# Kernel optimization log

Measured on AMD Instinct MI355X. Metric: run time of the kernel, lower is better.

The kernel has to match this reference:

```python
import jax, jax.numpy as jnp
import numpy as np

PC_RANGE = (-50.0, -50.0, -4.0, 50.0, 50.0, 4.0)
IMG_H, IMG_W = 256.0, 704.0
EPS = 1e-5


def _bilinear_sample(feat, u, v):
    # feat [H,W,C]; u,v [M] in [0,1]; matches F.grid_sample(align_corners=False, padding_mode='zeros')
    H, W, _ = feat.shape
    x = u * W - 0.5
    y = v * H - 0.5
    x0 = jnp.floor(x)
    y0 = jnp.floor(y)
    dx = (x - x0)[:, None]
    dy = (y - y0)[:, None]
    x0 = x0.astype(jnp.int32)
    y0 = y0.astype(jnp.int32)

    def g(xi, yi):
        inb = ((xi >= 0) & (xi < W) & (yi >= 0) & (yi < H)).astype(feat.dtype)[:, None]
        return feat[jnp.clip(yi, 0, H - 1), jnp.clip(xi, 0, W - 1)] * inb

    return (g(x0, y0) * (1 - dx) * (1 - dy) + g(x0 + 1, y0) * dx * (1 - dy)
            + g(x0, y0 + 1) * (1 - dx) * dy + g(x0 + 1, y0 + 1) * dx * dy)


def _conv1x1(t, w, b):
    return jnp.einsum('bchw,oc->bohw', t, w) + b[None, :, None, None]


def _inorm(t, eps=1e-5):
    # InstanceNorm2d (affine=False): normalize per (b, c) over spatial dims
    m = t.mean(axis=(2, 3), keepdims=True)
    var = t.var(axis=(2, 3), keepdims=True)
    return (t - m) * jax.lax.rsqrt(var + eps)


def _forward(feat, lidar2img, bev_pos, pe_w1, pe_b1, pe_w2, pe_b2, pe_w3, pe_b3,
             c1_w, c1_b, c2_w, c2_b, c3_w, c3_b):
    B, N, C, Hf, Wf = feat.shape
    _, P, Hb, Wb, _ = bev_pos.shape
    Q = Hb * Wb
    lo = jnp.asarray(PC_RANGE[:3], feat.dtype)
    hi = jnp.asarray(PC_RANGE[3:], feat.dtype)
    # 'b p h w d -> b (h w) p d', then scale normalized coords into pc_range
    ref01 = jnp.transpose(bev_pos, (0, 2, 3, 1, 4)).reshape(B, Q, P, 3)
    ref = ref01 * (hi - lo) + lo
    # project through per-camera lidar2img (homogeneous)
    pts = jnp.concatenate([ref, jnp.ones_like(ref[..., :1])], axis=-1)  # [B,Q,P,4]
    cam = jnp.einsum('bnij,bqpj->bnqpi', lidar2img, pts)                # [B,N,Q,P,4]
    homo = cam[..., 2]
    z = jnp.maximum(homo, EPS)
    u = cam[..., 0] / z / IMG_W
    v = cam[..., 1] / z / IMG_H
    valid = ((homo > EPS) & (u > 0.0) & (u < 1.0) & (v > 0.0) & (v < 1.0)).astype(feat.dtype)
    # bilinear gather per camera; feats to channel-last ('b n (g c) h w -> (b g) n h w c', G=1)
    fmap = jnp.transpose(feat, (0, 1, 3, 4, 2)).reshape(B * N, Hf, Wf, C)
    samp = jax.vmap(_bilinear_sample)(fmap, u.reshape(B * N, Q * P), v.reshape(B * N, Q * P))
    samp = samp.reshape(B, N, Q, P, C) * valid[..., None]
    samp = samp.sum(axis=1)  # sum over cameras -> [B,Q,P,C]
    # PositionalEncodingMap(3 -> 256 -> 256 -> 128) on normalized reference points
    pe = jax.nn.relu(ref01 @ pe_w1 + pe_b1)
    pe = jax.nn.relu(pe @ pe_w2 + pe_b2)
    pe = pe @ pe_w3 + pe_b3
    samp = samp + pe
    # 'b (h w) g p c -> b (p g c) h w' with g=1
    x = jnp.transpose(samp.reshape(B, Hb, Wb, P, C), (0, 3, 4, 1, 2)).reshape(B, P * C, Hb, Wb)
    gelu = lambda t: jax.nn.gelu(t, approximate=False)
    x = gelu(_inorm(_conv1x1(x, c1_w, c1_b)))
    x = gelu(_inorm(_conv1x1(x, c2_w, c2_b)))
    x = _conv1x1(x, c3_w, c3_b)
    return x


def setup_inputs() -> dict:
    key = jax.random.key(0)
    ks = jax.random.split(key, 16)
    B, N, C, Hf, Wf = 1, 6, 128, 32, 88
    P, Hb, Wb = 4, 160, 160
    E = 128
    MID = 256
    s = 0.02
    return {
        'feat': jax.random.normal(ks[0], (B, N, C, Hf, Wf), jnp.float32),
        'lidar2img': jax.random.normal(ks[1], (B, N, 4, 4), jnp.float32),
        'bev_pos': jax.random.uniform(ks[2], (B, P, Hb, Wb, 3), jnp.float32),
        'pe_w1': jax.random.normal(ks[3], (3, MID), jnp.float32) * s,
        'pe_b1': jnp.zeros((MID,), jnp.float32),
        'pe_w2': jax.random.normal(ks[4], (MID, MID), jnp.float32) * s,
        'pe_b2': jnp.zeros((MID,), jnp.float32),
        'pe_w3': jax.random.normal(ks[5], (MID, E), jnp.float32) * s,
        'pe_b3': jnp.zeros((E,), jnp.float32),
        'c1_w': jax.random.normal(ks[6], (4 * E, P * 128), jnp.float32) * s,
        'c1_b': jnp.zeros((4 * E,), jnp.float32),
        'c2_w': jax.random.normal(ks[7], (E, 4 * E), jnp.float32) * s,
        'c2_b': jnp.zeros((E,), jnp.float32),
        'c3_w': jax.random.normal(ks[8], (E, E), jnp.float32) * s,
        'c3_b': jnp.zeros((E,), jnp.float32),
    }


def reference(feat, lidar2img, bev_pos, pe_w1, pe_b1, pe_w2, pe_b2, pe_w3, pe_b3,
              c1_w, c1_b, c2_w, c2_b, c3_w, c3_b):
    return _forward(feat, lidar2img, bev_pos, pe_w1, pe_b1, pe_w2, pe_b2, pe_w3, pe_b3,
                    c1_w, c1_b, c2_w, c2_b, c3_w, c3_b)
```

## Files before the change

kernel.cpp:

```cpp
#include <hip/hip_runtime.h>
#include <cstdint>
#include <cstddef>

using frag8 = __attribute__((ext_vector_type(8))) short;
using f32x4 = __attribute__((ext_vector_type(4))) float;

__device__ __forceinline__ float b2f_bits(unsigned short u) {
    union { uint32_t u32; float f; } x; x.u32 = ((uint32_t)u) << 16; return x.f;
}
__device__ __forceinline__ float b2f_lo(uint32_t pk) {
    return __builtin_bit_cast(float, pk << 16);
}
__device__ __forceinline__ float b2f_hi(uint32_t pk) {
    return __builtin_bit_cast(float, pk & 0xffff0000u);
}
__device__ __forceinline__ unsigned short f2b(float f) {
    uint32_t u = __builtin_bit_cast(uint32_t, f);
    uint32_t r = (u + 0x7fffu + ((u >> 16) & 1u)) >> 16;
    return (unsigned short)r;
}

#define HF 32
#define WFEAT 88
#define NCAM 6
#define NPT 102400
#define BM 128
#define BN 128
#define BK 64

__global__ __launch_bounds__(256) void k_prep(const float* __restrict__ feat,
                                              const float* __restrict__ pw2,
                                              const float* __restrict__ pw3,
                                              const float* __restrict__ c1w,
                                              const float* __restrict__ c2w,
                                              const float* __restrict__ c3w,
                                              const float* __restrict__ pw1,
                                              const float* __restrict__ pb1,
                                              const float* __restrict__ l2i,
                                              const float* __restrict__ bev,
                                              unsigned short* __restrict__ featT,
                                              unsigned short* __restrict__ W2Tb,
                                              unsigned short* __restrict__ W3Tb,
                                              unsigned short* __restrict__ C1Wb,
                                              unsigned short* __restrict__ C2Wb,
                                              unsigned short* __restrict__ C3Wb,
                                              unsigned short* __restrict__ H1,
                                              float* __restrict__ stats,
                                              int* __restrict__ poff,
                                              float4* __restrict__ pwts) {
    __shared__ unsigned short tile[64 * 132];
    int b = blockIdx.x, t = threadIdx.x;
    if (b < 25600) {
        int idx = b * 256 + t;
        int m = idx >> 6;
        int o4 = (idx & 63) * 4;
        int q = m >> 2, p = m & 3;
        int h = q / 160, w = q - h * 160;
        const float* bv = bev + ((p * 160 + h) * 160 + w) * 3;
        float cx = bv[0], cy = bv[1], cz = bv[2];
        float4 a0 = *(const float4*)(pw1 + o4);
        float4 a1 = *(const float4*)(pw1 + 256 + o4);
        float4 a2 = *(const float4*)(pw1 + 512 + o4);
        float4 bb = *(const float4*)(pb1 + o4);
        ushort4 o;
        o.x = f2b(fmaxf(cx * a0.x + cy * a1.x + cz * a2.x + bb.x, 0.f));
        o.y = f2b(fmaxf(cx * a0.y + cy * a1.y + cz * a2.y + bb.y, 0.f));
        o.z = f2b(fmaxf(cx * a0.z + cy * a1.z + cz * a2.z + bb.z, 0.f));
        o.w = f2b(fmaxf(cx * a0.w + cy * a1.w + cz * a2.w + bb.w, 0.f));
        *(ushort4*)(H1 + (size_t)m * 256 + o4) = o;
        return;
    }
    b -= 25600;
    if (b < 2400) {
        int idx = b * 256 + t;
        int n = idx / NPT, pt = idx - n * NPT;
        int q = pt >> 2, p = pt & 3;
        int h = q / 160, w = q - h * 160;
        const float* bv = bev + ((p * 160 + h) * 160 + w) * 3;
        float rx = bv[0] * 100.f - 50.f;
        float ry = bv[1] * 100.f - 50.f;
        float rz = bv[2] * 8.f - 4.f;
        const float* M = l2i + n * 16;
        float c0   = M[0] * rx + M[1] * ry + M[2]  * rz + M[3];
        float c1v  = M[4] * rx + M[5] * ry + M[6]  * rz + M[7];
        float homo = M[8] * rx + M[9] * ry + M[10] * rz + M[11];
        float z = fmaxf(homo, 1e-5f);
        float u = c0 / z / 704.0f;
        float v = c1v / z / 256.0f;
        if (!(homo > 1e-5f && u > 0.f && u < 1.f && v > 0.f && v < 1.f)) {
            poff[idx] = -1;
            return;
        }
        float fx = u * (float)WFEAT - 0.5f;
        float fy = v * (float)HF - 0.5f;
        float fx0 = floorf(fx), fy0 = floorf(fy);
        float dx = fx - fx0, dy = fy - fy0;
        int x0 = (int)fx0, y0 = (int)fy0;
        float wxa = (x0 < 0) ? dx : 1.f - dx;
        float wxb = (x0 >= 0 && x0 < WFEAT - 1) ? dx : 0.f;
        float wya = (y0 < 0) ? dy : 1.f - dy;
        float wyb = (y0 >= 0 && y0 < HF - 1) ? dy : 0.f;
        int bx = max(x0, 0), by = max(y0, 0);
        poff[idx] = ((n * HF + by) * WFEAT + bx) << 7;
        pwts[idx] = make_float4(wxa * wya, wxb * wya, wxa * wyb, wxb * wyb);
        return;
    }
    b -= 2400;
    if (b < 264) {
        int n = b / 44;
        int s0 = (b - n * 44) * 64;
        #pragma unroll
        for (int i = 0; i < 32; ++i) {
            int e = i * 256 + t;
            int c = e >> 6, sl = e & 63;
            tile[sl * 132 + c] = f2b(feat[(size_t)(n * 128 + c) * 2816 + s0 + sl]);
        }
        __syncthreads();
        #pragma unroll
        for (int j = 0; j < 8; ++j) {
            int flat = j * 1024 + t * 4;
            int sl = flat >> 7, c = flat & 127;
            ushort4 v = *(const ushort4*)(tile + sl * 132 + c);
            *(ushort4*)(featT + (size_t)(n * 2816 + s0 + sl) * 128 + c) = v;
        }
        return;
    }
    b -= 264;
    if (b < 256) {
        int idx = b * 256 + t;
        int r = idx >> 8, c = idx & 255;
        W2Tb[c * 256 + r] = f2b(pw2[idx]);
        return;
    }
    b -= 256;
    if (b < 128) {
        int idx = b * 256 + t;
        int r = idx >> 7, c = idx & 127;
        W3Tb[c * 128 + 0] = W3Tb[c * 128];
        W3Tb[c * 256 + r] = f2b(pw3[idx]);
        return;
    }
    b -= 128;
    if (b < 1024) { int idx = b * 256 + t; C1Wb[idx] = f2b(c1w[idx]); return; }
    b -= 1024;
    if (b < 256)  { int idx = b * 256 + t; C2Wb[idx] = f2b(c2w[idx]); return; }
    b -= 256;
    if (b < 64)   { int idx = b * 256 + t; C3Wb[idx] = f2b(c3w[idx]); return; }
    #pragma unroll
    for (int j = 0; j < 10; ++j) stats[t * 10 + j] = 0.f;
}

__global__ __launch_bounds__(256) void k_sample2(const unsigned short* __restrict__ featT,
                                                 const int* __restrict__ poff,
                                                 const float4* __restrict__ pwts,
                                                 unsigned short* __restrict__ samp) {
    int pt = blockIdx.x * 4 + (threadIdx.x >> 6);
    int lane = threadIdx.x & 63;
    int c2 = lane * 2;
    int offs[NCAM];
    float4 ww[NCAM];
    #pragma unroll
    for (int n = 0; n < NCAM; ++n) offs[n] = poff[n * NPT + pt];
    #pragma unroll
    for (int n = 0; n < NCAM; ++n) ww[n] = pwts[n * NPT + pt];
    float acc0 = 0.f, acc1 = 0.f;
    #pragma unroll
    for (int n = 0; n < NCAM; ++n) {
        if (offs[n] >= 0) {
            const unsigned short* base = featT + offs[n] + c2;
            uint32_t p00 = *(const uint32_t*)(base);
            uint32_t p01 = *(const uint32_t*)(base + 128);
            uint32_t p10 = *(const uint32_t*)(base + WFEAT * 128);
            uint32_t p11 = *(const uint32_t*)(base + WFEAT * 128 + 128);
            float4 w = ww[n];
            acc0 += w.x * b2f_lo(p00) + w.y * b2f_lo(p01) + w.z * b2f_lo(p10) + w.w * b2f_lo(p11);
            acc1 += w.x * b2f_hi(p00) + w.y * b2f_hi(p01) + w.z * b2f_hi(p10) + w.w * b2f_hi(p11);
        }
    }
    uint32_t outpk = (uint32_t)f2b(acc0) | ((uint32_t)f2b(acc1) << 16);
    *(uint32_t*)(samp + (size_t)pt * 128 + c2) = outpk;
}

__device__ __forceinline__ void stage_tile_big(const unsigned short* __restrict__ g, int ld,
                                               unsigned short* lds, int t) {
    int r = t >> 2, cs = t & 3;
    int cl = cs ^ ((r >> 1) & 3);
    __builtin_amdgcn_global_load_lds(
        (const __attribute__((address_space(1))) void*)(g + (size_t)r * ld + cl * 8),
        (__attribute__((address_space(3))) void*)(lds + (t >> 6) * 512),
        16, 0, 0);
}

__device__ __forceinline__ frag8 frag_read_big(const unsigned short* lds, int row, int chunk) {
    return *(const frag8*)(lds + row * 32 + ((chunk ^ ((row >> 1) & 3)) << 3));
}

__device__ __forceinline__ void mma_tile_big(const unsigned short* As, const unsigned short* Bs,
                                             int wm, int wn, int lane, f32x4 (&acc)[4][4]) {
    int lm = lane & 15, lq = lane >> 4;
    frag8 a[4], b[4];
    #pragma unroll
    for (int t = 0; t < 4; ++t) a[t] = frag_read_big(As, wm * 64 + t * 16 + lm, lq);
    #pragma unroll
    for (int t = 0; t < 4; ++t) b[t] = frag_read_big(Bs, wn * 64 + t * 16 + lm, lq);
    #pragma unroll
    for (int tm = 0; tm < 4; ++tm)
        #pragma unroll
        for (int tn = 0; tn < 4; ++tn)
            acc[tm][tn] = __builtin_amdgcn_mfma_f32_16x16x32_bf16(a[tm], b[tn], acc[tm][tn], 0, 0, 0);
}

template <int KT>
__device__ __forceinline__ void gemm_loop_big(const unsigned short* __restrict__ A, int ldA,
                                              const unsigned short* __restrict__ B, int ldB,
                                              unsigned short (*As)[256 * 32],
                                              unsigned short (*Bs)[256 * 32],
                                              int t, int wm, int wn, int lane,
                                              f32x4 (&acc)[4][4]) {
    stage_tile_big(A, ldA, As[0], t);
    stage_tile_big(B, ldB, Bs[0], t);
    __syncthreads();
    #pragma unroll
    for (int kt = 0; kt < KT; ++kt) {
        int cur = kt & 1, nxt = cur ^ 1;
        if (kt + 1 < KT) {
            stage_tile_big(A + (kt + 1) * 32, ldA, As[nxt], t);
            stage_tile_big(B + (kt + 1) * 32, ldB, Bs[nxt], t);
        }
        mma_tile_big(As[cur], Bs[cur], wm, wn, lane, acc);
        __syncthreads();
    }
}

__global__ __launch_bounds__(1024) void k_gemm_pe2_big(const unsigned short* __restrict__ A,
                                                       const unsigned short* __restrict__ Bt,
                                                       const float* __restrict__ bias,
                                                       unsigned short* __restrict__ H2) {
    __shared__ unsigned short As[2][256 * 32], Bs[2][256 * 32];
    int t = threadIdx.x, lane = t & 63, wid = t >> 6;
    int wm = wid >> 2, wn = wid & 3;
    int m0 = blockIdx.x * 256;
    f32x4 acc[4][4] = {};
    gemm_loop_big<8>(A + (size_t)m0 * 256, 256, Bt, 256, As, Bs, t, wm, wn, lane, acc);
    int lm = lane & 15, lq = lane >> 4;
    #pragma unroll
    for (int tn = 0; tn < 4; ++tn) {
        int n = wn * 64 + tn * 16 + lm;
        float bn = bias[n];
        #pragma unroll
        for (int tm = 0; tm < 4; ++tm) {
            int mb = m0 + wm * 64 + tm * 16 + lq * 4;
            #pragma unroll
            for (int rr = 0; rr < 4; ++rr)
                H2[(size_t)(mb + rr) * 256 + n] = f2b(fmaxf(acc[tm][tn][rr] + bn, 0.f));
        }
    }
}

__global__ __launch_bounds__(1024) void k_gemm_conv1_big(const unsigned short* __restrict__ A,
                                                         const unsigned short* __restrict__ Bt,
                                                         const float* __restrict__ bias,
                                                         unsigned short* __restrict__ Y,
                                                         float* __restrict__ st) {
    __shared__ unsigned short As[2][256 * 32], Bs[2][256 * 32];
    int t = threadIdx.x, lane = t & 63, wid = t >> 6;
    int wm = wid >> 2, wn = wid & 3;
    int m0 = blockIdx.x * 256, n0 = blockIdx.y * 256;
    f32x4 acc[4][4] = {};
    gemm_loop_big<16>(A + (size_t)m0 * 512, 512, Bt + (size_t)n0 * 512, 512,
                      As, Bs, t, wm, wn, lane, acc);
    int lm = lane & 15, lq = lane >> 4;
    #pragma unroll
    for (int tn = 0; tn < 4; ++tn) {
        int n = n0 + wn * 64 + tn * 16 + lm;
        float bn = bias[n];
        float s1 = 0.f, s2 = 0.f;
        #pragma unroll
        for (int tm = 0; tm < 4; ++tm) {
            int mb = m0 + wm * 64 + tm * 16 + lq * 4;
            #pragma unroll
            for (int rr = 0; rr < 4; ++rr) {
                float v = acc[tm][tn][rr] + bn;
                Y[(size_t)(mb + rr) * 512 + n] = f2b(v);
                s1 += v; s2 += v * v;
            }
        }
        s1 += __shfl_xor(s1, 16); s1 += __shfl_xor(s1, 32);
        s2 += __shfl_xor(s2, 16); s2 += __shfl_xor(s2, 32);
        if (lq == 0) { atomicAdd(&st[n], s1); atomicAdd(&st[512 + n], s2); }
    }
}

__device__ __forceinline__ void stage_tile(const unsigned short* __restrict__ g, int ld,
                                           unsigned short* lds, int wave, int lane) {
    #pragma unroll
    for (int j = 0; j < 4; ++j) {
        int idx = wave * 256 + j * 64 + lane;
        int r = idx >> 3;
        int cs = idx & 7;
        int cl = cs ^ (r & 7);
        __builtin_amdgcn_global_load_lds(
            (const __attribute__((address_space(1))) void*)(g + (size_t)r * ld + cl * 8),
            (__attribute__((address_space(3))) void*)(lds + wave * 2048 + j * 512),
            16, 0, 0);
    }
}

__device__ __forceinline__ frag8 frag_read(const unsigned short* lds, int row, int chunk) {
    return *(const frag8*)(lds + row * 64 + ((chunk ^ (row & 7)) << 3));
}

__device__ __forceinline__ void mma_tile(const unsigned short* As, const unsigned short* Bs,
                                         int wm, int wn, int lane, f32x4 (&acc)[4][4]) {
    int lm = lane & 15, lq = lane >> 4;
    #pragma unroll
    for (int kk = 0; kk < 2; ++kk) {
        frag8 a[4], b[4];
        #pragma unroll
        for (int t = 0; t < 4; ++t) a[t] = frag_read(As, wm * 64 + t * 16 + lm, kk * 4 + lq);
        #pragma unroll
        for (int t = 0; t < 4; ++t) b[t] = frag_read(Bs, wn * 64 + t * 16 + lm, kk * 4 + lq);
        #pragma unroll
        for (int tm = 0; tm < 4; ++tm)
            #pragma unroll
            for (int tn = 0; tn < 4; ++tn)
                acc[tm][tn] = __builtin_amdgcn_mfma_f32_16x16x32_bf16(a[tm], b[tn], acc[tm][tn], 0, 0, 0);
    }
}

__global__ __launch_bounds__(256) void k_gemm_pe3(const unsigned short* __restrict__ A,
                                                  const unsigned short* __restrict__ Bt,
                                                  const float* __restrict__ bias,
                                                  const unsigned short* __restrict__ samp,
                                                  unsigned short* __restrict__ X) {
    __shared__ unsigned short As[BM * BK], Bs[BN * BK];
    int lane = threadIdx.x & 63, wave = threadIdx.x >> 6;
    int wm = wave >> 1, wn = wave & 1;
    int m0 = blockIdx.x * BM;
    f32x4 acc[4][4] = {};
    for (int kt = 0; kt < 4; ++kt) {
        stage_tile(A + (size_t)m0 * 256 + kt * BK, 256, As, wave, lane);
        stage_tile(Bt + (size_t)kt * BK, 256, Bs, wave, lane);
        __syncthreads();
        mma_tile(As, Bs, wm, wn, lane, acc);
        __syncthreads();
    }
    int lm = lane & 15, lq = lane >> 4;
    #pragma unroll
    for (int tn = 0; tn < 4; ++tn) {
        int n = wn * 64 + tn * 16 + lm;
        float bn = bias[n];
        #pragma unroll
        for (int tm = 0; tm < 4; ++tm) {
            int mb = m0 + wm * 64 + tm * 16 + lq * 4;
            #pragma unroll
            for (int rr = 0; rr < 4; ++rr) {
                size_t off = (size_t)(mb + rr) * 128 + n;
                X[off] = f2b(acc[tm][tn][rr] + bn + b2f_bits(samp[off]));
            }
        }
    }
}

template <int K, bool STATS>
__global__ __launch_bounds__(256) void k_gemm_conv(const unsigned short* __restrict__ A,
                                                   const unsigned short* __restrict__ Bt,
                                                   const float* __restrict__ bias,
                                                   unsigned short* __restrict__ Y, int ldY,
                                                   float* __restrict__ st, int C) {
    __shared__ unsigned short As[BM * BK], Bs[BN * BK];
    int lane = threadIdx.x & 63, wave = threadIdx.x >> 6;
    int wm = wave >> 1, wn = wave & 1;
    int m0 = blockIdx.x * BM, n0 = blockIdx.y * BN;
    f32x4 acc[4][4] = {};
    for (int kt = 0; kt < K / BK; ++kt) {
        stage_tile(A + (size_t)m0 * K + kt * BK, K, As, wave, lane);
        stage_tile(Bt + (size_t)n0 * K + kt * BK, K, Bs, wave, lane);
        __syncthreads();
        mma_tile(As, Bs, wm, wn, lane, acc);
        __syncthreads();
    }
    int lm = lane & 15, lq = lane >> 4;
    #pragma unroll
    for (int tn = 0; tn < 4; ++tn) {
        int n = n0 + wn * 64 + tn * 16 + lm;
        float bn = bias[n];
        float s1 = 0.f, s2 = 0.f;
        #pragma unroll
        for (int tm = 0; tm < 4; ++tm) {
            int mb = m0 + wm * 64 + tm * 16 + lq * 4;
            #pragma unroll
            for (int rr = 0; rr < 4; ++rr) {
                float v = acc[tm][tn][rr] + bn;
                Y[(size_t)(mb + rr) * ldY + n] = f2b(v);
                if (STATS) { s1 += v; s2 += v * v; }
            }
        }
        if (STATS) {
            s1 += __shfl_xor(s1, 16); s1 += __shfl_xor(s1, 32);
            s2 += __shfl_xor(s2, 16); s2 += __shfl_xor(s2, 32);
            if (lq == 0) { atomicAdd(&st[n], s1); atomicAdd(&st[C + n], s2); }
        }
    }
}

__global__ __launch_bounds__(256) void k_gemm_conv3(const unsigned short* __restrict__ A,
                                                    const unsigned short* __restrict__ Bt,
                                                    const float* __restrict__ bias,
                                                    float* __restrict__ out) {
    __shared__ unsigned short As[BM * BK], Bs[BN * BK];
    int lane = threadIdx.x & 63, wave = threadIdx.x >> 6;
    int wm = wave >> 1, wn = wave & 1;
    int m0 = blockIdx.x * BM;
    f32x4 acc[4][4] = {};
    for (int kt = 0; kt < 2; ++kt) {
        stage_tile(A + (size_t)m0 * 128 + kt * BK, 128, As, wave, lane);
        stage_tile(Bt + (size_t)kt * BK, 128, Bs, wave, lane);
        __syncthreads();
        mma_tile(As, Bs, wm, wn, lane, acc);
        __syncthreads();
    }
    int lm = lane & 15, lq = lane >> 4;
    #pragma unroll
    for (int tn = 0; tn < 4; ++tn) {
        int n = wn * 64 + tn * 16 + lm;
        float bn = bias[n];
        #pragma unroll
        for (int tm = 0; tm < 4; ++tm) {
            int mb = m0 + wm * 64 + tm * 16 + lq * 4;
            float4 pk;
            pk.x = acc[tm][tn][0] + bn;
            pk.y = acc[tm][tn][1] + bn;
            pk.z = acc[tm][tn][2] + bn;
            pk.w = acc[tm][tn][3] + bn;
            *(float4*)(out + (size_t)n * 25600 + mb) = pk;
        }
    }
}

__global__ void k_normgelu8f(const unsigned short* __restrict__ Y, const float* __restrict__ st,
                             unsigned short* __restrict__ X2, int Cmask, int C, float inv_n,
                             int total8) {
    int i8 = blockIdx.x * 256 + threadIdx.x;
    if (i8 >= total8) return;
    int e0 = i8 * 8;
    int c = e0 & Cmask;
    uint4 y = *(const uint4*)(Y + e0);
    float4 s1a = *(const float4*)(st + c);
    float4 s1b = *(const float4*)(st + c + 4);
    float4 s2a = *(const float4*)(st + C + c);
    float4 s2b = *(const float4*)(st + C + c + 4);
    float mu[8] = { s1a.x * inv_n, s1a.y * inv_n, s1a.z * inv_n, s1a.w * inv_n,
                    s1b.x * inv_n, s1b.y * inv_n, s1b.z * inv_n, s1b.w * inv_n };
    float sq[8] = { s2a.x, s2a.y, s2a.z, s2a.w, s2b.x, s2b.y, s2b.z, s2b.w };
    float rs[8];
    #pragma unroll
    for (int j = 0; j < 8; ++j) rs[j] = rsqrtf(sq[j] * inv_n - mu[j] * mu[j] + 1e-5f);
    const float is2 = 0.70710678118654752f;
    unsigned int yw[4] = {y.x, y.y, y.z, y.w};
    unsigned int ow[4];
    #pragma unroll
    for (int j = 0; j < 4; ++j) {
        float v0 = (b2f_bits((unsigned short)(yw[j] & 0xffffu)) - mu[j * 2]) * rs[j * 2];
        float v1 = (b2f_bits((unsigned short)(yw[j] >> 16)) - mu[j * 2 + 1]) * rs[j * 2 + 1];
        float g0 = 0.5f * v0 * (1.f + erff(v0 * is2));
        float g1 = 0.5f * v1 * (1.f + erff(v1 * is2));
        ow[j] = (uint32_t)f2b(g0) | ((uint32_t)f2b(g1) << 16);
    }
    *(uint4*)(X2 + e0) = make_uint4(ow[0], ow[1], ow[2], ow[3]);
}

extern "C" void kernel_launch(void* const* d_in, const int* in_sizes, int n_in,
                              void* d_out, int out_size, void* d_ws, size_t ws_size,
                              hipStream_t stream) {
    (void)in_sizes; (void)n_in; (void)out_size; (void)ws_size;
    const float* feat = (const float*)d_in[0];
    const float* l2i  = (const float*)d_in[1];
    const float* bev  = (const float*)d_in[2];
    const float* pw1  = (const float*)d_in[3];
    const float* pb1  = (const float*)d_in[4];
    const float* pw2  = (const float*)d_in[5];
    const float* pb2  = (const float*)d_in[6];
    const float* pw3  = (const float*)d_in[7];
    const float* pb3  = (const float*)d_in[8];
    const float* c1w  = (const float*)d_in[9];
    const float* c1b  = (const float*)d_in[10];
    const float* c2w  = (const float*)d_in[11];
    const float* c2b  = (const float*)d_in[12];
    const float* c3w  = (const float*)d_in[13];
    const float* c3b  = (const float*)d_in[14];
    float* outp = (float*)d_out;
    char* ws = (char*)d_ws;

    unsigned short* featT = (unsigned short*)(ws + 0);
    unsigned short* W2Tb  = (unsigned short*)(ws + 4348416);
    unsigned short* W3Tb  = (unsigned short*)(ws + 4479488);
    unsigned short* C1Wb  = (unsigned short*)(ws + 4545024);
    unsigned short* C2Wb  = (unsigned short*)(ws + 5069312);
    unsigned short* C3Wb  = (unsigned short*)(ws + 5200384);
    float* stats          = (float*)(ws + 5233152);
    int*    poff          = (int*)(ws + 5247488);
    float4* pwts          = (float4*)(ws + 7705088);
    char* BUF1 = ws + 17535488;
    char* BUF2 = ws + 69964288;
    char* BUF3 = ws + 122393088;

    float* st512 = stats;
    float* st128 = stats + 2048;

    unsigned short* H1   = (unsigned short*)BUF1;
    unsigned short* H2   = (unsigned short*)BUF2;
    unsigned short* samp = (unsigned short*)BUF3;
    unsigned short* X    = (unsigned short*)BUF1;
    unsigned short* Y1   = (unsigned short*)BUF2;
    unsigned short* X2   = (unsigned short*)BUF3;
    unsigned short* Y2   = (unsigned short*)BUF1;
    unsigned short* X3   = (unsigned short*)(BUF1 + 6553600);

    k_prep<<<29993, 256, 0, stream>>>(feat, pw2, pw3, c1w, c2w, c3w, pw1, pb1, l2i, bev,
                                      featT, W2Tb, W3Tb, C1Wb, C2Wb, C3Wb, H1, stats,
                                      poff, pwts);

    k_sample2<<<25600, 256, 0, stream>>>(featT, poff, pwts, samp);

    k_gemm_pe2_big<<<400, 1024, 0, stream>>>(H1, W2Tb, pb2, H2);
    k_gemm_pe3<<<dim3(800, 1), 256, 0, stream>>>(H2, W3Tb, pb3, samp, X);

    k_gemm_conv1_big<<<dim3(100, 2), 1024, 0, stream>>>(X, C1Wb, c1b, Y1, st512);
    k_normgelu8f<<<6400, 256, 0, stream>>>(Y1, st512, X2, 511, 512, 1.f / 25600.f, 1638400);

    k_gemm_conv<512, true><<<dim3(200, 1), 256, 0, stream>>>(X2, C2Wb, c2b, Y2, 128, st128, 128);
    k_normgelu8f<<<1600, 256, 0, stream>>>(Y2, st128, X3, 127, 128, 1.f / 25600.f, 409600);

    k_gemm_conv3<<<dim3(200, 1), 256, 0, stream>>>(X3, C3Wb, c3b, outp);
}
```

Measured before the change: 280.2 us.

## Fuse PE layer-2 and layer-3 GEMMs, keeping the hidden tile in LDS

Merges the second and third positional-encoding GEMMs into one kernel. The ReLU'd H2 tile goes to padded shared memory, which reuses the staging buffers through a union, and the third GEMM reads W3 fragments straight from global memory. This removes the H2 round trip through global memory and one kernel launch. Buffer assignments are reshuffled to match, and a stray self-assignment in weight prep is removed. The third GEMM loads W3 from global memory without staging, and the 260-wide LDS rows may cause bank conflicts.

```diff
diff --git a/kernel.cpp b/kernel.cpp
--- a/kernel.cpp
+++ b/kernel.cpp
@@ -136,7 +136,6 @@
     if (b < 128) {
         int idx = b * 256 + t;
         int r = idx >> 7, c = idx & 127;
-        W3Tb[c * 128 + 0] = W3Tb[c * 128];
         W3Tb[c * 256 + r] = f2b(pw3[idx]);
         return;
     }
@@ -232,27 +231,67 @@
     }
 }
 
-__global__ __launch_bounds__(1024) void k_gemm_pe2_big(const unsigned short* __restrict__ A,
-                                                       const unsigned short* __restrict__ Bt,
-                                                       const float* __restrict__ bias,
-                                                       unsigned short* __restrict__ H2) {
-    __shared__ unsigned short As[2][256 * 32], Bs[2][256 * 32];
+__global__ __launch_bounds__(1024) void k_gemm_pe23(const unsigned short* __restrict__ A,
+                                                    const unsigned short* __restrict__ W2,
+                                                    const float* __restrict__ b2,
+                                                    const unsigned short* __restrict__ W3,
+                                                    const float* __restrict__ b3,
+                                                    const unsigned short* __restrict__ samp,
+                                                    unsigned short* __restrict__ X) {
+    __shared__ union {
+        struct { unsigned short As[2][256 * 32]; unsigned short Bs[2][256 * 32]; } s;
+        unsigned short h2[256 * 260];
+    } u;
     int t = threadIdx.x, lane = t & 63, wid = t >> 6;
     int wm = wid >> 2, wn = wid & 3;
     int m0 = blockIdx.x * 256;
+    int lm = lane & 15, lq = lane >> 4;
+
     f32x4 acc[4][4] = {};
-    gemm_loop_big<8>(A + (size_t)m0 * 256, 256, Bt, 256, As, Bs, t, wm, wn, lane, acc);
-    int lm = lane & 15, lq = lane >> 4;
+    gemm_loop_big<8>(A + (size_t)m0 * 256, 256, W2, 256, u.s.As, u.s.Bs, t, wm, wn, lane, acc);
     #pragma unroll
     for (int tn = 0; tn < 4; ++tn) {
         int n = wn * 64 + tn * 16 + lm;
-        float bn = bias[n];
+        float bn = b2[n];
+        #pragma unroll
+        for (int tm = 0; tm < 4; ++tm) {
+            int rb = wm * 64 + tm * 16 + lq * 4;
+            #pragma unroll
+            for (int rr = 0; rr < 4; ++rr)
+                u.h2[(rb + rr) * 260 + n] = f2b(fmaxf(acc[tm][tn][rr] + bn, 0.f));
+        }
+    }
+    __syncthreads();
+
+    f32x4 acc2[4][2] = {};
+    const unsigned short* w3p0 = W3 + (size_t)(wn * 32 + lm) * 256 + lq * 8;
+    const unsigned short* w3p1 = w3p0 + 16 * 256;
+    #pragma unroll
+    for (int kt = 0; kt < 8; ++kt) {
+        frag8 b0 = *(const frag8*)(w3p0 + kt * 32);
+        frag8 b1 = *(const frag8*)(w3p1 + kt * 32);
+        frag8 a[4];
+        #pragma unroll
+        for (int tm = 0; tm < 4; ++tm)
+            a[tm] = *(const frag8*)(&u.h2[(wm * 64 + tm * 16 + lm) * 260 + kt * 32 + lq * 8]);
+        #pragma unroll
+        for (int tm = 0; tm < 4; ++tm) {
+            acc2[tm][0] = __builtin_amdgcn_mfma_f32_16x16x32_bf16(a[tm], b0, acc2[tm][0], 0, 0, 0);
+            acc2[tm][1] = __builtin_amdgcn_mfma_f32_16x16x32_bf16(a[tm], b1, acc2[tm][1], 0, 0, 0);
+        }
+    }
+    #pragma unroll
+    for (int tn = 0; tn < 2; ++tn) {
+        int n = wn * 32 + tn * 16 + lm;
+        float bn = b3[n];
         #pragma unroll
         for (int tm = 0; tm < 4; ++tm) {
             int mb = m0 + wm * 64 + tm * 16 + lq * 4;
             #pragma unroll
-            for (int rr = 0; rr < 4; ++rr)
-                H2[(size_t)(mb + rr) * 256 + n] = f2b(fmaxf(acc[tm][tn][rr] + bn, 0.f));
+            for (int rr = 0; rr < 4; ++rr) {
+                size_t off = (size_t)(mb + rr) * 128 + n;
+                X[off] = f2b(acc2[tm][tn][rr] + bn + b2f_bits(samp[off]));
+            }
         }
     }
 }
@@ -325,40 +364,6 @@
             #pragma unroll
             for (int tn = 0; tn < 4; ++tn)
                 acc[tm][tn] = __builtin_amdgcn_mfma_f32_16x16x32_bf16(a[tm], b[tn], acc[tm][tn], 0, 0, 0);
-    }
-}
-
-__global__ __launch_bounds__(256) void k_gemm_pe3(const unsigned short* __restrict__ A,
-                                                  const unsigned short* __restrict__ Bt,
-                                                  const float* __restrict__ bias,
-                                                  const unsigned short* __restrict__ samp,
-                                                  unsigned short* __restrict__ X) {
-    __shared__ unsigned short As[BM * BK], Bs[BN * BK];
-    int lane = threadIdx.x & 63, wave = threadIdx.x >> 6;
-    int wm = wave >> 1, wn = wave & 1;
-    int m0 = blockIdx.x * BM;
-    f32x4 acc[4][4] = {};
-    for (int kt = 0; kt < 4; ++kt) {
-        stage_tile(A + (size_t)m0 * 256 + kt * BK, 256, As, wave, lane);
-        stage_tile(Bt + (size_t)kt * BK, 256, Bs, wave, lane);
-        __syncthreads();
-        mma_tile(As, Bs, wm, wn, lane, acc);
-        __syncthreads();
-    }
-    int lm = lane & 15, lq = lane >> 4;
-    #pragma unroll
-    for (int tn = 0; tn < 4; ++tn) {
-        int n = wn * 64 + tn * 16 + lm;
-        float bn = bias[n];
-        #pragma unroll
-        for (int tm = 0; tm < 4; ++tm) {
-            int mb = m0 + wm * 64 + tm * 16 + lq * 4;
-            #pragma unroll
-            for (int rr = 0; rr < 4; ++rr) {
-                size_t off = (size_t)(mb + rr) * 128 + n;
-                X[off] = f2b(acc[tm][tn][rr] + bn + b2f_bits(samp[off]));
-            }
-        }
     }
 }
 
@@ -509,13 +514,12 @@
     float* st128 = stats + 2048;
 
     unsigned short* H1   = (unsigned short*)BUF1;
-    unsigned short* H2   = (unsigned short*)BUF2;
     unsigned short* samp = (unsigned short*)BUF3;
-    unsigned short* X    = (unsigned short*)BUF1;
-    unsigned short* Y1   = (unsigned short*)BUF2;
+    unsigned short* X    = (unsigned short*)BUF2;
+    unsigned short* Y1   = (unsigned short*)BUF1;
     unsigned short* X2   = (unsigned short*)BUF3;
-    unsigned short* Y2   = (unsigned short*)BUF1;
-    unsigned short* X3   = (unsigned short*)(BUF1 + 6553600);
+    unsigned short* Y2   = (unsigned short*)BUF2;
+    unsigned short* X3   = (unsigned short*)BUF1;
 
     k_prep<<<29993, 256, 0, stream>>>(feat, pw2, pw3, c1w, c2w, c3w, pw1, pb1, l2i, bev,
                                       featT, W2Tb, W3Tb, C1Wb, C2Wb, C3Wb, H1, stats,
@@ -523,8 +527,7 @@
 
     k_sample2<<<25600, 256, 0, stream>>>(featT, poff, pwts, samp);
 
-    k_gemm_pe2_big<<<400, 1024, 0, stream>>>(H1, W2Tb, pb2, H2);
-    k_gemm_pe3<<<dim3(800, 1), 256, 0, stream>>>(H2, W3Tb, pb3, samp, X);
+    k_gemm_pe23<<<400, 1024, 0, stream>>>(H1, W2Tb, pb2, W3Tb, pb3, samp, X);
 
     k_gemm_conv1_big<<<dim3(100, 2), 1024, 0, stream>>>(X, C1Wb, c1b, Y1, st512);
     k_normgelu8f<<<6400, 256, 0, stream>>>(Y1, st512, X2, 511, 512, 1.f / 25600.f, 1638400);
```

New measurement: 289.9 us. 1.03x slower.

## Merge bilinear sampling and PE layer-2 GEMM into one interleaved launch

Applied to the files above, without the earlier changes.

Replaces the separate sampling kernel and the large 1024-thread PE2 GEMM with a single launch. Blocks are interleaved so that every 17th block does a 128x128 GEMM tile while the other 16 do gather-based sampling. The aim is to overlap memory-bound gathers with MFMA compute and remove one launch. The cost is that the GEMM now uses smaller tiles without double buffering, and its 16 KB LDS allocation also applies to the sampling blocks, which may limit occupancy. A redundant self-copy store in the weight prep is also removed.

```diff
diff --git a/kernel.cpp b/kernel.cpp
--- a/kernel.cpp
+++ b/kernel.cpp
@@ -136,7 +136,6 @@
     if (b < 128) {
         int idx = b * 256 + t;
         int r = idx >> 7, c = idx & 127;
-        W3Tb[c * 128 + 0] = W3Tb[c * 128];
         W3Tb[c * 256 + r] = f2b(pw3[idx]);
         return;
     }
@@ -150,35 +149,106 @@
     for (int j = 0; j < 10; ++j) stats[t * 10 + j] = 0.f;
 }
 
-__global__ __launch_bounds__(256) void k_sample2(const unsigned short* __restrict__ featT,
-                                                 const int* __restrict__ poff,
-                                                 const float4* __restrict__ pwts,
-                                                 unsigned short* __restrict__ samp) {
-    int pt = blockIdx.x * 4 + (threadIdx.x >> 6);
-    int lane = threadIdx.x & 63;
-    int c2 = lane * 2;
-    int offs[NCAM];
-    float4 ww[NCAM];
-    #pragma unroll
-    for (int n = 0; n < NCAM; ++n) offs[n] = poff[n * NPT + pt];
-    #pragma unroll
-    for (int n = 0; n < NCAM; ++n) ww[n] = pwts[n * NPT + pt];
-    float acc0 = 0.f, acc1 = 0.f;
-    #pragma unroll
-    for (int n = 0; n < NCAM; ++n) {
-        if (offs[n] >= 0) {
-            const unsigned short* base = featT + offs[n] + c2;
-            uint32_t p00 = *(const uint32_t*)(base);
-            uint32_t p01 = *(const uint32_t*)(base + 128);
-            uint32_t p10 = *(const uint32_t*)(base + WFEAT * 128);
-            uint32_t p11 = *(const uint32_t*)(base + WFEAT * 128 + 128);
-            float4 w = ww[n];
-            acc0 += w.x * b2f_lo(p00) + w.y * b2f_lo(p01) + w.z * b2f_lo(p10) + w.w * b2f_lo(p11);
-            acc1 += w.x * b2f_hi(p00) + w.y * b2f_hi(p01) + w.z * b2f_hi(p10) + w.w * b2f_hi(p11);
-        }
-    }
-    uint32_t outpk = (uint32_t)f2b(acc0) | ((uint32_t)f2b(acc1) << 16);
-    *(uint32_t*)(samp + (size_t)pt * 128 + c2) = outpk;
+__device__ __forceinline__ void stage_tile(const unsigned short* __restrict__ g, int ld,
+                                           unsigned short* lds, int wave, int lane) {
+    #pragma unroll
+    for (int j = 0; j < 4; ++j) {
+        int idx = wave * 256 + j * 64 + lane;
+        int r = idx >> 3;
+        int cs = idx & 7;
+        int cl = cs ^ (r & 7);
+        __builtin_amdgcn_global_load_lds(
+            (const __attribute__((address_space(1))) void*)(g + (size_t)r * ld + cl * 8),
+            (__attribute__((address_space(3))) void*)(lds + wave * 2048 + j * 512),
+            16, 0, 0);
+    }
+}
+
+__device__ __forceinline__ frag8 frag_read(const unsigned short* lds, int row, int chunk) {
+    return *(const frag8*)(lds + row * 64 + ((chunk ^ (row & 7)) << 3));
+}
+
+__device__ __forceinline__ void mma_tile(const unsigned short* As, const unsigned short* Bs,
+                                         int wm, int wn, int lane, f32x4 (&acc)[4][4]) {
+    int lm = lane & 15, lq = lane >> 4;
+    #pragma unroll
+    for (int kk = 0; kk < 2; ++kk) {
+        frag8 a[4], b[4];
+        #pragma unroll
+        for (int t = 0; t < 4; ++t) a[t] = frag_read(As, wm * 64 + t * 16 + lm, kk * 4 + lq);
+        #pragma unroll
+        for (int t = 0; t < 4; ++t) b[t] = frag_read(Bs, wn * 64 + t * 16 + lm, kk * 4 + lq);
+        #pragma unroll
+        for (int tm = 0; tm < 4; ++tm)
+            #pragma unroll
+            for (int tn = 0; tn < 4; ++tn)
+                acc[tm][tn] = __builtin_amdgcn_mfma_f32_16x16x32_bf16(a[tm], b[tn], acc[tm][tn], 0, 0, 0);
+    }
+}
+
+__global__ __launch_bounds__(256) void k_samp_pe2(const unsigned short* __restrict__ featT,
+                                                  const int* __restrict__ poff,
+                                                  const float4* __restrict__ pwts,
+                                                  unsigned short* __restrict__ samp,
+                                                  const unsigned short* __restrict__ H1,
+                                                  const unsigned short* __restrict__ W2,
+                                                  const float* __restrict__ b2,
+                                                  unsigned short* __restrict__ H2) {
+    __shared__ unsigned short As[BM * BK], Bs[BN * BK];
+    int b = blockIdx.x;
+    int g = b / 17, r = b - g * 17;
+    if (r < 16) {
+        int pt = (g * 16 + r) * 4 + (threadIdx.x >> 6);
+        int lane = threadIdx.x & 63;
+        int c2 = lane * 2;
+        int offs[NCAM];
+        float4 ww[NCAM];
+        #pragma unroll
+        for (int n = 0; n < NCAM; ++n) offs[n] = poff[n * NPT + pt];
+        #pragma unroll
+        for (int n = 0; n < NCAM; ++n) ww[n] = pwts[n * NPT + pt];
+        float acc0 = 0.f, acc1 = 0.f;
+        #pragma unroll
+        for (int n = 0; n < NCAM; ++n) {
+            if (offs[n] >= 0) {
+                const unsigned short* base = featT + offs[n] + c2;
+                uint32_t p00 = *(const uint32_t*)(base);
+                uint32_t p01 = *(const uint32_t*)(base + 128);
+                uint32_t p10 = *(const uint32_t*)(base + WFEAT * 128);
+                uint32_t p11 = *(const uint32_t*)(base + WFEAT * 128 + 128);
+                float4 w = ww[n];
+                acc0 += w.x * b2f_lo(p00) + w.y * b2f_lo(p01) + w.z * b2f_lo(p10) + w.w * b2f_lo(p11);
+                acc1 += w.x * b2f_hi(p00) + w.y * b2f_hi(p01) + w.z * b2f_hi(p10) + w.w * b2f_hi(p11);
+            }
+        }
+        uint32_t outpk = (uint32_t)f2b(acc0) | ((uint32_t)f2b(acc1) << 16);
+        *(uint32_t*)(samp + (size_t)pt * 128 + c2) = outpk;
+        return;
+    }
+    int lane = threadIdx.x & 63, wave = threadIdx.x >> 6;
+    int wm = wave >> 1, wn = wave & 1;
+    int m0 = (g >> 1) * BM, n0 = (g & 1) * BN;
+    f32x4 acc[4][4] = {};
+    for (int kt = 0; kt < 4; ++kt) {
+        stage_tile(H1 + (size_t)m0 * 256 + kt * BK, 256, As, wave, lane);
+        stage_tile(W2 + (size_t)n0 * 256 + kt * BK, 256, Bs, wave, lane);
+        __syncthreads();
+        mma_tile(As, Bs, wm, wn, lane, acc);
+        __syncthreads();
+    }
+    int lm = lane & 15, lq = lane >> 4;
+    #pragma unroll
+    for (int tn = 0; tn < 4; ++tn) {
+        int n = n0 + wn * 64 + tn * 16 + lm;
+        float bn = b2[n];
+        #pragma unroll
+        for (int tm = 0; tm < 4; ++tm) {
+            int mb = m0 + wm * 64 + tm * 16 + lq * 4;
+            #pragma unroll
+            for (int rr = 0; rr < 4; ++rr)
+                H2[(size_t)(mb + rr) * 256 + n] = f2b(fmaxf(acc[tm][tn][rr] + bn, 0.f));
+        }
+    }
 }
 
 __device__ __forceinline__ void stage_tile_big(const unsigned short* __restrict__ g, int ld,
@@ -229,31 +299,6 @@
         }
         mma_tile_big(As[cur], Bs[cur], wm, wn, lane, acc);
         __syncthreads();
-    }
-}
-
-__global__ __launch_bounds__(1024) void k_gemm_pe2_big(const unsigned short* __restrict__ A,
-                                                       const unsigned short* __restrict__ Bt,
-                                                       const float* __restrict__ bias,
-                                                       unsigned short* __restrict__ H2) {
-    __shared__ unsigned short As[2][256 * 32], Bs[2][256 * 32];
-    int t = threadIdx.x, lane = t & 63, wid = t >> 6;
-    int wm = wid >> 2, wn = wid & 3;
-    int m0 = blockIdx.x * 256;
-    f32x4 acc[4][4] = {};
-    gemm_loop_big<8>(A + (size_t)m0 * 256, 256, Bt, 256, As, Bs, t, wm, wn, lane, acc);
-    int lm = lane & 15, lq = lane >> 4;
-    #pragma unroll
-    for (int tn = 0; tn < 4; ++tn) {
-        int n = wn * 64 + tn * 16 + lm;
-        float bn = bias[n];
-        #pragma unroll
-        for (int tm = 0; tm < 4; ++tm) {
-            int mb = m0 + wm * 64 + tm * 16 + lq * 4;
-            #pragma unroll
-            for (int rr = 0; rr < 4; ++rr)
-                H2[(size_t)(mb + rr) * 256 + n] = f2b(fmaxf(acc[tm][tn][rr] + bn, 0.f));
-        }
     }
 }
 
@@ -288,43 +333,6 @@
         s1 += __shfl_xor(s1, 16); s1 += __shfl_xor(s1, 32);
         s2 += __shfl_xor(s2, 16); s2 += __shfl_xor(s2, 32);
         if (lq == 0) { atomicAdd(&st[n], s1); atomicAdd(&st[512 + n], s2); }
-    }
-}
-
-__device__ __forceinline__ void stage_tile(const unsigned short* __restrict__ g, int ld,
-                                           unsigned short* lds, int wave, int lane) {
-    #pragma unroll
-    for (int j = 0; j < 4; ++j) {
-        int idx = wave * 256 + j * 64 + lane;
-        int r = idx >> 3;
-        int cs = idx & 7;
-        int cl = cs ^ (r & 7);
-        __builtin_amdgcn_global_load_lds(
-            (const __attribute__((address_space(1))) void*)(g + (size_t)r * ld + cl * 8),
-            (__attribute__((address_space(3))) void*)(lds + wave * 2048 + j * 512),
-            16, 0, 0);
-    }
-}
-
-__device__ __forceinline__ frag8 frag_read(const unsigned short* lds, int row, int chunk) {
-    return *(const frag8*)(lds + row * 64 + ((chunk ^ (row & 7)) << 3));
-}
-
-__device__ __forceinline__ void mma_tile(const unsigned short* As, const unsigned short* Bs,
-                                         int wm, int wn, int lane, f32x4 (&acc)[4][4]) {
-    int lm = lane & 15, lq = lane >> 4;
-    #pragma unroll
-    for (int kk = 0; kk < 2; ++kk) {
-        frag8 a[4], b[4];
-        #pragma unroll
-        for (int t = 0; t < 4; ++t) a[t] = frag_read(As, wm * 64 + t * 16 + lm, kk * 4 + lq);
-        #pragma unroll
-        for (int t = 0; t < 4; ++t) b[t] = frag_read(Bs, wn * 64 + t * 16 + lm, kk * 4 + lq);
-        #pragma unroll
-        for (int tm = 0; tm < 4; ++tm)
-            #pragma unroll
-            for (int tn = 0; tn < 4; ++tn)
-                acc[tm][tn] = __builtin_amdgcn_mfma_f32_16x16x32_bf16(a[tm], b[tn], acc[tm][tn], 0, 0, 0);
     }
 }
 
@@ -521,9 +529,8 @@
                                       featT, W2Tb, W3Tb, C1Wb, C2Wb, C3Wb, H1, stats,
                                       poff, pwts);
 
-    k_sample2<<<25600, 256, 0, stream>>>(featT, poff, pwts, samp);
-
-    k_gemm_pe2_big<<<400, 1024, 0, stream>>>(H1, W2Tb, pb2, H2);
+    k_samp_pe2<<<27200, 256, 0, stream>>>(featT, poff, pwts, samp, H1, W2Tb, pb2, H2);
+
     k_gemm_pe3<<<dim3(800, 1), 256, 0, stream>>>(H2, W3Tb, pb3, samp, X);
 
     k_gemm_conv1_big<<<dim3(100, 2), 1024, 0, stream>>>(X, C1Wb, c1b, Y1, st512);
```

New measurement: 300.2 us. 1.07x slower.

## Replace pe3 GEMM with 1024-thread double-buffered 256-row tile kernel

Applied to the files above, without the earlier changes.

Swaps the 256-thread pe3 GEMM (128-row tiles, 800 blocks, single-buffered LDS staging) for a 1024-thread kernel that computes 256x128 output tiles. It double-buffers the A and B tiles in LDS using direct global-to-LDS loads, with the 128-row B tile loaded redundantly by two halves of the block. The aim is more A reuse per block and hiding load latency behind the MFMA work. It also drops a stray redundant self-copy write in the weight-transpose prep. The cost is only 400 blocks, each holding more LDS, and duplicated B-load traffic.

```diff
diff --git a/kernel.cpp b/kernel.cpp
--- a/kernel.cpp
+++ b/kernel.cpp
@@ -136,7 +136,6 @@
     if (b < 128) {
         int idx = b * 256 + t;
         int r = idx >> 7, c = idx & 127;
-        W3Tb[c * 128 + 0] = W3Tb[c * 128];
         W3Tb[c * 256 + r] = f2b(pw3[idx]);
         return;
     }
@@ -191,6 +190,17 @@
         16, 0, 0);
 }
 
+__device__ __forceinline__ void stage_tile_128dup(const unsigned short* __restrict__ g, int ld,
+                                                  unsigned short* lds, int t) {
+    int tt = t & 511;
+    int r = tt >> 2, cs = tt & 3;
+    int cl = cs ^ ((r >> 1) & 3);
+    __builtin_amdgcn_global_load_lds(
+        (const __attribute__((address_space(1))) void*)(g + (size_t)r * ld + cl * 8),
+        (__attribute__((address_space(3))) void*)(lds + (tt >> 6) * 512),
+        16, 0, 0);
+}
+
 __device__ __forceinline__ frag8 frag_read_big(const unsigned short* lds, int row, int chunk) {
     return *(const frag8*)(lds + row * 32 + ((chunk ^ ((row >> 1) & 3)) << 3));
 }
@@ -253,6 +263,56 @@
             #pragma unroll
             for (int rr = 0; rr < 4; ++rr)
                 H2[(size_t)(mb + rr) * 256 + n] = f2b(fmaxf(acc[tm][tn][rr] + bn, 0.f));
+        }
+    }
+}
+
+__global__ __launch_bounds__(1024) void k_gemm_pe3_big(const unsigned short* __restrict__ A,
+                                                       const unsigned short* __restrict__ Bt,
+                                                       const float* __restrict__ bias,
+                                                       const unsigned short* __restrict__ samp,
+                                                       unsigned short* __restrict__ X) {
+    __shared__ unsigned short As[2][256 * 32], Bs[2][128 * 32];
+    int t = threadIdx.x, lane = t & 63, wid = t >> 6;
+    int wm = wid >> 2, wn = wid & 3;
+    int m0 = blockIdx.x * 256;
+    int lm = lane & 15, lq = lane >> 4;
+    const unsigned short* Ab = A + (size_t)m0 * 256;
+    f32x4 acc[4][2] = {};
+    stage_tile_big(Ab, 256, As[0], t);
+    stage_tile_128dup(Bt, 256, Bs[0], t);
+    __syncthreads();
+    #pragma unroll
+    for (int kt = 0; kt < 8; ++kt) {
+        int cur = kt & 1, nxt = cur ^ 1;
+        if (kt + 1 < 8) {
+            stage_tile_big(Ab + (kt + 1) * 32, 256, As[nxt], t);
+            stage_tile_128dup(Bt + (kt + 1) * 32, 256, Bs[nxt], t);
+        }
+        frag8 a[4], b[2];
+        #pragma unroll
+        for (int tm = 0; tm < 4; ++tm) a[tm] = frag_read_big(As[cur], wm * 64 + tm * 16 + lm, lq);
+        #pragma unroll
+        for (int tn = 0; tn < 2; ++tn) b[tn] = frag_read_big(Bs[cur], wn * 32 + tn * 16 + lm, lq);
+        #pragma unroll
+        for (int tm = 0; tm < 4; ++tm) {
+            acc[tm][0] = __builtin_amdgcn_mfma_f32_16x16x32_bf16(a[tm], b[0], acc[tm][0], 0, 0, 0);
+            acc[tm][1] = __builtin_amdgcn_mfma_f32_16x16x32_bf16(a[tm], b[1], acc[tm][1], 0, 0, 0);
+        }
+        __syncthreads();
+    }
+    #pragma unroll
+    for (int tn = 0; tn < 2; ++tn) {
+        int n = wn * 32 + tn * 16 + lm;
+        float bn = bias[n];
+        #pragma unroll
+        for (int tm = 0; tm < 4; ++tm) {
+            int mb = m0 + wm * 64 + tm * 16 + lq * 4;
+            #pragma unroll
+            for (int rr = 0; rr < 4; ++rr) {
+                size_t off = (size_t)(mb + rr) * 128 + n;
+                X[off] = f2b(acc[tm][tn][rr] + bn + b2f_bits(samp[off]));
+            }
         }
     }
 }
@@ -325,40 +385,6 @@
             #pragma unroll
             for (int tn = 0; tn < 4; ++tn)
                 acc[tm][tn] = __builtin_amdgcn_mfma_f32_16x16x32_bf16(a[tm], b[tn], acc[tm][tn], 0, 0, 0);
-    }
-}
-
-__global__ __launch_bounds__(256) void k_gemm_pe3(const unsigned short* __restrict__ A,
-                                                  const unsigned short* __restrict__ Bt,
-                                                  const float* __restrict__ bias,
-                                                  const unsigned short* __restrict__ samp,
-                                                  unsigned short* __restrict__ X) {
-    __shared__ unsigned short As[BM * BK], Bs[BN * BK];
-    int lane = threadIdx.x & 63, wave = threadIdx.x >> 6;
-    int wm = wave >> 1, wn = wave & 1;
-    int m0 = blockIdx.x * BM;
-    f32x4 acc[4][4] = {};
-    for (int kt = 0; kt < 4; ++kt) {
-        stage_tile(A + (size_t)m0 * 256 + kt * BK, 256, As, wave, lane);
-        stage_tile(Bt + (size_t)kt * BK, 256, Bs, wave, lane);
-        __syncthreads();
-        mma_tile(As, Bs, wm, wn, lane, acc);
-        __syncthreads();
-    }
-    int lm = lane & 15, lq = lane >> 4;
-    #pragma unroll
-    for (int tn = 0; tn < 4; ++tn) {
-        int n = wn * 64 + tn * 16 + lm;
-        float bn = bias[n];
-        #pragma unroll
-        for (int tm = 0; tm < 4; ++tm) {
-            int mb = m0 + wm * 64 + tm * 16 + lq * 4;
-            #pragma unroll
-            for (int rr = 0; rr < 4; ++rr) {
-                size_t off = (size_t)(mb + rr) * 128 + n;
-                X[off] = f2b(acc[tm][tn][rr] + bn + b2f_bits(samp[off]));
-            }
-        }
     }
 }
 
@@ -524,7 +550,7 @@
     k_sample2<<<25600, 256, 0, stream>>>(featT, poff, pwts, samp);
 
     k_gemm_pe2_big<<<400, 1024, 0, stream>>>(H1, W2Tb, pb2, H2);
-    k_gemm_pe3<<<dim3(800, 1), 256, 0, stream>>>(H2, W3Tb, pb3, samp, X);
+    k_gemm_pe3_big<<<400, 1024, 0, stream>>>(H2, W3Tb, pb3, samp, X);
 
     k_gemm_conv1_big<<<dim3(100, 2), 1024, 0, stream>>>(X, C1Wb, c1b, Y1, st512);
     k_normgelu8f<<<6400, 256, 0, stream>>>(Y1, st512, X2, 511, 512, 1.f / 25600.f, 1638400);
```

New measurement: 282.4 us. Within noise of the previous version (+0.8%).
